# Performance work log

Hardware: AMD Instinct MI355X
Metric: run time of the kernel (lower is better)

Reference implementation:

```python
import jax, jax.numpy as jnp
import numpy as np

N_NODES = 100000


def gcn_conv(x, src, dst, dinv, W, b):
    # PyG GCNConv: h = D^-1/2 (A+I) D^-1/2 (x W) + b
    h = x @ W                                   # [N, out]
    norm = dinv[src] * dinv[dst]                # [E'] edge weights
    msg = norm[:, None] * h[src]                # gather + scale
    agg = jax.ops.segment_sum(msg, dst, num_segments=x.shape[0])
    return agg + b


def setup_inputs() -> dict:
    key = jax.random.key(0)
    ks = jax.random.split(key, 8)
    x = jax.random.normal(ks[0], (N_NODES, 64), dtype=jnp.float32)
    edge_index = jax.random.randint(ks[1], (2, 1600000), 0, N_NODES, dtype=jnp.int32)
    s = 0.1
    return {
        "x": x,
        "edge_index": edge_index,
        "W1": jax.random.normal(ks[2], (64, 64), dtype=jnp.float32) * s,
        "b1": jnp.zeros((64,), dtype=jnp.float32),
        "W2": jax.random.normal(ks[3], (64, 32), dtype=jnp.float32) * s,
        "b2": jnp.zeros((32,), dtype=jnp.float32),
        "W3": jax.random.normal(ks[4], (32, 2), dtype=jnp.float32) * s,
        "b3": jnp.zeros((2,), dtype=jnp.float32),
    }


def reference(x, edge_index, W1, b1, W2, b2, W3, b3):
    n = x.shape[0]
    loop = jnp.arange(n, dtype=edge_index.dtype)
    src = jnp.concatenate([edge_index[0], loop])  # add self-loops
    dst = jnp.concatenate([edge_index[1], loop])
    deg = jax.ops.segment_sum(jnp.ones_like(dst, dtype=x.dtype), dst, num_segments=n)
    dinv = jnp.where(deg > 0, jax.lax.rsqrt(jnp.maximum(deg, 1.0)), 0.0)
    h = jax.nn.relu(gcn_conv(x, src, dst, dinv, W1, b1))
    h = jax.nn.relu(gcn_conv(h, src, dst, dinv, W2, b2))
    return gcn_conv(h, src, dst, dinv, W3, b3)
```

## Files before the change

kernel.cpp:

```cpp
#include <hip/hip_runtime.h>
#include <hip/hip_fp16.h>

#define N_NODES 100000
#define N_EDGES 1600000
#define BSHIFT 9
#define NBUCK ((N_NODES + 511) / 512)
#define BCAP 12288

__global__ void bucket1_kernel(const int* __restrict__ src, const int* __restrict__ dst,
                               int* __restrict__ gbcount, int* __restrict__ bbuf, int E) {
    __shared__ int hcnt[NBUCK];
    __shared__ int hbase[NBUCK];
    int t = threadIdx.x;
    for (int i = t; i < NBUCK; i += 256) hcnt[i] = 0;
    __syncthreads();
    int e0 = blockIdx.x * 2048 + t;
    int ss[8], dd[8];
#pragma unroll
    for (int u = 0; u < 8; u++) {
        int e = e0 + u * 256;
        if (e < E) {
            ss[u] = src[e];
            dd[u] = dst[e];
            atomicAdd(&hcnt[dd[u] >> BSHIFT], 1);
        } else {
            dd[u] = -1;
        }
    }
    __syncthreads();
    for (int i = t; i < NBUCK; i += 256) {
        int c = hcnt[i];
        hbase[i] = c ? atomicAdd(&gbcount[i], c) : 0;
        hcnt[i] = 0;
    }
    __syncthreads();
#pragma unroll
    for (int u = 0; u < 8; u++) {
        if (dd[u] >= 0) {
            int bk = dd[u] >> BSHIFT;
            int r = atomicAdd(&hcnt[bk], 1);
            bbuf[(size_t)bk * BCAP + hbase[bk] + r] = ss[u] | ((dd[u] & 511) << 17);
        }
    }
}

__global__ void scan196_kernel(const int* __restrict__ gbcount, int* __restrict__ gbase,
                               int* __restrict__ rowptrN, int E) {
    __shared__ int s[256];
    int t = threadIdx.x;
    int v = (t < NBUCK) ? gbcount[t] : 0;
    s[t] = v;
    __syncthreads();
    for (int off = 1; off < 256; off <<= 1) {
        int u = (t >= off) ? s[t - off] : 0;
        __syncthreads();
        s[t] += u;
        __syncthreads();
    }
    if (t < NBUCK) gbase[t] = s[t] - v;
    if (t == 0) *rowptrN = E;
}

__global__ __launch_bounds__(512)
void bucket2_kernel(const int* __restrict__ bbuf, const int* __restrict__ gbcount,
                    const int* __restrict__ gbase, int* __restrict__ rowptr,
                    float* __restrict__ dinv, int* __restrict__ eidx, int N) {
    int b = blockIdx.x;
    int base_node = b << BSHIFT;
    int nn = min(512, N - base_node);
    int t = threadIdx.x;
    __shared__ int s[512];
    __shared__ int cur[512];
    s[t] = 0;
    __syncthreads();
    int sz = gbcount[b];
    const int* eb = bbuf + (size_t)b * BCAP;
    for (int j = t; j < sz; j += 512) atomicAdd(&s[((unsigned)eb[j]) >> 17], 1);
    __syncthreads();
    int myc = s[t];
    if (t < nn) dinv[base_node + t] = rsqrtf((float)myc + 1.0f);
    __syncthreads();
    for (int off = 1; off < 512; off <<= 1) {
        int u = (t >= off) ? s[t - off] : 0;
        __syncthreads();
        s[t] += u;
        __syncthreads();
    }
    int rp = gbase[b] + s[t] - myc;
    if (t < nn) rowptr[base_node + t] = rp;
    cur[t] = rp;
    __syncthreads();
    for (int j = t; j < sz; j += 512) {
        int e = eb[j];
        int pos = atomicAdd(&cur[((unsigned)e) >> 17], 1);
        eidx[pos] = e & 0x1FFFF;
    }
}

__global__ void sortrow_wave(const int* __restrict__ rowptr, int* __restrict__ eidx, int n) {
    int g = (blockIdx.x * blockDim.x + threadIdx.x) >> 6;
    int lane = threadIdx.x & 63;
    if (g >= n) return;
    int start = rowptr[g];
    int end = rowptr[g + 1];
    int len = end - start;
    if (len <= 1) return;

    if (len <= 64) {
        int v = (lane < len) ? eidx[start + lane] : 0x7fffffff;
#pragma unroll
        for (int k = 2; k <= 64; k <<= 1) {
#pragma unroll
            for (int j = k >> 1; j > 0; j >>= 1) {
                int partner = __shfl_xor(v, j, 64);
                bool up = ((lane & k) == 0);
                bool keepMin = (((lane & j) == 0) == up);
                int mn = min(v, partner), mx = max(v, partner);
                v = keepMin ? mn : mx;
            }
        }
        if (lane < len) eidx[start + lane] = v;
    } else if (lane == 0) {
        for (int i = start + 1; i < end; i++) {
            int key = eidx[i];
            int j = i - 1;
            while (j >= start && eidx[j] > key) { eidx[j + 1] = eidx[j]; j--; }
            eidx[j + 1] = key;
        }
    }
}

template <int FIN, int FOUT>
__global__ __launch_bounds__(256, 2)
void gemm_tiled(const float* __restrict__ in, const float* __restrict__ W,
                const float* __restrict__ dinv, __half* __restrict__ out, int n) {
    constexpr int CG = FOUT / 4;
    constexpr int RG = 256 / CG;
    constexpr int TR = RG * 4;
    constexpr int LDA = FIN + 4;
    __shared__ float sIn[TR * LDA];
    __shared__ float sW[FIN * FOUT];

    for (int i = threadIdx.x; i < FIN * FOUT / 4; i += 256)
        ((float4*)sW)[i] = ((const float4*)W)[i];

    int r0 = blockIdx.x * TR;
    for (int i = threadIdx.x; i < TR * FIN / 4; i += 256) {
        int rr = i / (FIN / 4);
        int cc = i % (FIN / 4);
        int gr = r0 + rr;
        float4 v = (gr < n) ? ((const float4*)in)[(size_t)gr * (FIN / 4) + cc]
                            : make_float4(0.f, 0.f, 0.f, 0.f);
        *(float4*)&sIn[rr * LDA + cc * 4] = v;
    }
    __syncthreads();

    int tc = threadIdx.x % CG;
    int tr = threadIdx.x / CG;
    int rbase = tr * 4, cbase = tc * 4;
    float acc[4][4] = {};

#pragma unroll 2
    for (int k = 0; k < FIN; k += 4) {
        float4 a[4], b[4];
#pragma unroll
        for (int i = 0; i < 4; i++) a[i] = *(float4*)&sIn[(rbase + i) * LDA + k];
#pragma unroll
        for (int kk = 0; kk < 4; kk++) b[kk] = *(float4*)&sW[(k + kk) * FOUT + cbase];
#pragma unroll
        for (int i = 0; i < 4; i++) {
            acc[i][0] += a[i].x * b[0].x + a[i].y * b[1].x + a[i].z * b[2].x + a[i].w * b[3].x;
            acc[i][1] += a[i].x * b[0].y + a[i].y * b[1].y + a[i].z * b[2].y + a[i].w * b[3].y;
            acc[i][2] += a[i].x * b[0].z + a[i].y * b[1].z + a[i].z * b[2].z + a[i].w * b[3].z;
            acc[i][3] += a[i].x * b[0].w + a[i].y * b[1].w + a[i].z * b[2].w + a[i].w * b[3].w;
        }
    }

#pragma unroll
    for (int i = 0; i < 4; i++) {
        int gr = r0 + rbase + i;
        if (gr < n) {
            float dv = dinv[gr];
            union { __half h[4]; uint2 u; } pk;
            pk.h[0] = __float2half_rn(dv * acc[i][0]);
            pk.h[1] = __float2half_rn(dv * acc[i][1]);
            pk.h[2] = __float2half_rn(dv * acc[i][2]);
            pk.h[3] = __float2half_rn(dv * acc[i][3]);
            *(uint2*)&out[(size_t)gr * FOUT + cbase] = pk.u;
        }
    }
}

template <int FIN, int FOUT, bool OUT_HALF>
__global__ __launch_bounds__(256, 4)
void agg_gemm_kernel(const int* __restrict__ eidx, const int* __restrict__ rowptr,
                     const float* __restrict__ dinv, const __half* __restrict__ h,
                     const float* __restrict__ bias, const float* __restrict__ W,
                     void* __restrict__ outv, int n) {
    constexpr int L = 8;
    constexpr int PH = FIN / L;
    constexpr int NODES = 256 / L;
    constexpr int SVS = FIN + 1;
    using vh = _Float16 __attribute__((ext_vector_type(PH)));
    __shared__ float sW[FIN * FOUT];
    __shared__ float sv[NODES * SVS];

    for (int i = threadIdx.x; i < FIN * FOUT / 4; i += 256)
        ((float4*)sW)[i] = ((const float4*)W)[i];

    int g = (blockIdx.x * blockDim.x + threadIdx.x) / L;
    int lane = threadIdx.x % L;
    int slot = threadIdx.x / L;
    float di = 0.f;

    if (g < n) {
        int j = rowptr[g];
        int end = rowptr[g + 1];
        di = dinv[g];
        const __half* hb = h + lane * PH;

        float acc0[PH], acc1[PH];
#pragma unroll
        for (int q = 0; q < PH; q++) { acc0[q] = 0.f; acc1[q] = 0.f; }

        for (; j + 8 <= end; j += 8) {
            int s0 = eidx[j];
            int s1 = eidx[j + 1];
            int s2 = eidx[j + 2];
            int s3 = eidx[j + 3];
            int s4 = eidx[j + 4];
            int s5 = eidx[j + 5];
            int s6 = eidx[j + 6];
            int s7 = eidx[j + 7];
            vh v0 = *(const vh*)(hb + (size_t)s0 * FIN);
            vh v1 = *(const vh*)(hb + (size_t)s1 * FIN);
            vh v2 = *(const vh*)(hb + (size_t)s2 * FIN);
            vh v3 = *(const vh*)(hb + (size_t)s3 * FIN);
            vh v4 = *(const vh*)(hb + (size_t)s4 * FIN);
            vh v5 = *(const vh*)(hb + (size_t)s5 * FIN);
            vh v6 = *(const vh*)(hb + (size_t)s6 * FIN);
            vh v7 = *(const vh*)(hb + (size_t)s7 * FIN);
#pragma unroll
            for (int q = 0; q < PH; q++) {
                acc0[q] += (float)v0[q] + (float)v2[q];
                acc1[q] += (float)v1[q] + (float)v3[q];
                acc0[q] += (float)v4[q] + (float)v6[q];
                acc1[q] += (float)v5[q] + (float)v7[q];
            }
        }
        for (; j + 2 <= end; j += 2) {
            int s0 = eidx[j];
            int s1 = eidx[j + 1];
            vh v0 = *(const vh*)(hb + (size_t)s0 * FIN);
            vh v1 = *(const vh*)(hb + (size_t)s1 * FIN);
#pragma unroll
            for (int q = 0; q < PH; q++) { acc0[q] += (float)v0[q]; acc1[q] += (float)v1[q]; }
        }
        if (j < end) {
            vh v = *(const vh*)(hb + (size_t)eidx[j] * FIN);
#pragma unroll
            for (int q = 0; q < PH; q++) acc0[q] += (float)v[q];
        }

        vh sf = *(const vh*)(hb + (size_t)g * FIN);
        float* svn = &sv[slot * SVS + lane * PH];
#pragma unroll
        for (int q = 0; q < PH; q++) {
            float v = di * ((acc0[q] + acc1[q]) + (float)sf[q]) + bias[lane * PH + q];
            svn[q] = fmaxf(v, 0.f);
        }
    }
    __syncthreads();

    if (g < n) {
        const float* vn = &sv[slot * SVS];
        if constexpr (OUT_HALF) {
            constexpr int PC = FOUT / L;
            float o[PC] = {};
            for (int k = 0; k < FIN; k++) {
                float vk = vn[k];
                float4 w = *(const float4*)&sW[k * FOUT + lane * PC];
                o[0] += vk * w.x; o[1] += vk * w.y; o[2] += vk * w.z; o[3] += vk * w.w;
            }
            union { __half h[4]; uint2 u; } pk;
#pragma unroll
            for (int q = 0; q < PC; q++) pk.h[q] = __float2half_rn(di * o[q]);
            *(uint2*)((__half*)outv + (size_t)g * FOUT + lane * PC) = pk.u;
        } else {
            if (lane < FOUT) {
                float o = 0.f;
                for (int k = 0; k < FIN; k++) o += vn[k] * sW[k * FOUT + lane];
                ((float*)outv)[(size_t)g * FOUT + lane] = di * o;
            }
        }
    }
}

template <int F>
__global__ void agg_kernel(const int* __restrict__ eidx, const int* __restrict__ rowptr,
                           const float* __restrict__ dinv, const float* __restrict__ h,
                           const float* __restrict__ b, float* __restrict__ out, int n) {
    int g = (blockIdx.x * blockDim.x + threadIdx.x) / F;
    int lane = threadIdx.x % F;
    if (g >= n) return;
    int j = rowptr[g];
    int end = rowptr[g + 1];
    float di = dinv[g];
    float hs = h[(size_t)g * F + lane];

    float acc0 = 0.f, acc1 = 0.f, acc2 = 0.f, acc3 = 0.f;
    float acc4 = 0.f, acc5 = 0.f, acc6 = 0.f, acc7 = 0.f;
    for (; j + 8 <= end; j += 8) {
        int s0 = eidx[j];
        int s1 = eidx[j + 1];
        int s2 = eidx[j + 2];
        int s3 = eidx[j + 3];
        int s4 = eidx[j + 4];
        int s5 = eidx[j + 5];
        int s6 = eidx[j + 6];
        int s7 = eidx[j + 7];
        acc0 += h[(size_t)s0 * F + lane];
        acc1 += h[(size_t)s1 * F + lane];
        acc2 += h[(size_t)s2 * F + lane];
        acc3 += h[(size_t)s3 * F + lane];
        acc4 += h[(size_t)s4 * F + lane];
        acc5 += h[(size_t)s5 * F + lane];
        acc6 += h[(size_t)s6 * F + lane];
        acc7 += h[(size_t)s7 * F + lane];
    }
    for (; j + 2 <= end; j += 2) {
        int s0 = eidx[j];
        int s1 = eidx[j + 1];
        acc0 += h[(size_t)s0 * F + lane];
        acc1 += h[(size_t)s1 * F + lane];
    }
    if (j < end) {
        acc2 += h[(size_t)eidx[j] * F + lane];
    }
    float acc = ((acc0 + acc1) + (acc2 + acc3)) + ((acc4 + acc5) + (acc6 + acc7));
    out[(size_t)g * F + lane] = di * (acc + hs) + b[lane];
}

extern "C" void kernel_launch(void* const* d_in, const int* in_sizes, int n_in,
                              void* d_out, int out_size, void* d_ws, size_t ws_size,
                              hipStream_t stream) {
    const float* x  = (const float*)d_in[0];
    const int* ei   = (const int*)d_in[1];
    const float* W1 = (const float*)d_in[2];
    const float* b1 = (const float*)d_in[3];
    const float* W2 = (const float*)d_in[4];
    const float* b2 = (const float*)d_in[5];
    const float* W3 = (const float*)d_in[6];
    const float* b3 = (const float*)d_in[7];
    float* out = (float*)d_out;

    const int N = N_NODES;
    const int E = N_EDGES;
    const int* src = ei;
    const int* dst = ei + E;

    char* p = (char*)d_ws;
    int*    rowptr  = (int*)p;            p += ((size_t)(N + 1) * 4 + 15) / 16 * 16;
    float*  dinv    = (float*)p;          p += ((size_t)N * 4 + 15) / 16 * 16;
    int*    gbcount = (int*)p;            p += ((size_t)NBUCK * 4 + 15) / 16 * 16;
    int*    gbase   = (int*)p;            p += ((size_t)NBUCK * 4 + 15) / 16 * 16;
    int*    eidx    = (int*)p;            p += (size_t)E * 4;
    __half* A1      = (__half*)p;         p += (size_t)N * 64 * 2;
    __half* A2      = (__half*)p;         p += (size_t)N * 32 * 2;
    float*  A3      = (float*)p;          p += (size_t)N * 2 * 4;
    int*    bbuf    = (int*)p;

    const int T = 256;

    hipMemsetAsync(gbcount, 0, NBUCK * sizeof(int), stream);
    bucket1_kernel<<<(E + 2047) / 2048, T, 0, stream>>>(src, dst, gbcount, bbuf, E);
    scan196_kernel<<<1, 256, 0, stream>>>(gbcount, gbase, rowptr + N, E);
    bucket2_kernel<<<NBUCK, 512, 0, stream>>>(bbuf, gbcount, gbase, rowptr, dinv, eidx, N);
    sortrow_wave<<<(N * 64 + T - 1) / T, T, 0, stream>>>(rowptr, eidx, N);

    gemm_tiled<64, 64><<<(N + 63) / 64, T, 0, stream>>>(x, W1, dinv, A1, N);

    agg_gemm_kernel<64, 32, true><<<(N + 31) / 32, T, 0, stream>>>(
        eidx, rowptr, dinv, A1, b1, W2, A2, N);

    agg_gemm_kernel<32, 2, false><<<(N + 31) / 32, T, 0, stream>>>(
        eidx, rowptr, dinv, A2, b2, W3, A3, N);

    agg_kernel<2><<<(N * 2 + T - 1) / T, T, 0, stream>>>(eidx, rowptr, dinv, A3, b3, out, N);
}
```

Before: 266.8 us.

## Aggregate before first GEMM and fuse both layer GEMMs into one kernel

Uses associativity: layer 1 now aggregates dinv-scaled fp16 input features and applies W1 afterwards, instead of running a separate GEMM first. The x-to-fp16 conversion with dinv scaling is folded into bucket2, and a new kernel does aggregation, the W1 GEMM, bias plus ReLU, and the W2 GEMM in one pass. This drops the standalone gemm_tiled launch and one intermediate round trip. In exchange, x is rounded to fp16 before the matmul, and the new kernel holds more shared memory (W1+W2), which may lower occupancy.

```diff
diff --git a/kernel.cpp b/kernel.cpp
--- a/kernel.cpp
+++ b/kernel.cpp
@@ -64,13 +64,15 @@
 __global__ __launch_bounds__(512)
 void bucket2_kernel(const int* __restrict__ bbuf, const int* __restrict__ gbcount,
                     const int* __restrict__ gbase, int* __restrict__ rowptr,
-                    float* __restrict__ dinv, int* __restrict__ eidx, int N) {
+                    float* __restrict__ dinv, int* __restrict__ eidx,
+                    const float* __restrict__ x, __half* __restrict__ x16, int N) {
     int b = blockIdx.x;
     int base_node = b << BSHIFT;
     int nn = min(512, N - base_node);
     int t = threadIdx.x;
     __shared__ int s[512];
     __shared__ int cur[512];
+    __shared__ float sdinv[512];
     s[t] = 0;
     __syncthreads();
     int sz = gbcount[b];
@@ -78,7 +80,9 @@
     for (int j = t; j < sz; j += 512) atomicAdd(&s[((unsigned)eb[j]) >> 17], 1);
     __syncthreads();
     int myc = s[t];
-    if (t < nn) dinv[base_node + t] = rsqrtf((float)myc + 1.0f);
+    float dv = rsqrtf((float)myc + 1.0f);
+    sdinv[t] = dv;
+    if (t < nn) dinv[base_node + t] = dv;
     __syncthreads();
     for (int off = 1; off < 512; off <<= 1) {
         int u = (t >= off) ? s[t - off] : 0;
@@ -94,6 +98,17 @@
         int e = eb[j];
         int pos = atomicAdd(&cur[((unsigned)e) >> 17], 1);
         eidx[pos] = e & 0x1FFFF;
+    }
+    for (int i = t; i < nn * 16; i += 512) {
+        int r = i >> 4, c = i & 15;
+        float4 v = ((const float4*)x)[((size_t)(base_node + r)) * 16 + c];
+        float d = sdinv[r];
+        union { __half h[4]; uint2 u; } pk;
+        pk.h[0] = __float2half_rn(d * v.x);
+        pk.h[1] = __float2half_rn(d * v.y);
+        pk.h[2] = __float2half_rn(d * v.z);
+        pk.h[3] = __float2half_rn(d * v.w);
+        *(uint2*)&x16[((size_t)(base_node + r)) * 64 + c * 4] = pk.u;
     }
 }
 
@@ -130,64 +145,120 @@
     }
 }
 
-template <int FIN, int FOUT>
-__global__ __launch_bounds__(256, 2)
-void gemm_tiled(const float* __restrict__ in, const float* __restrict__ W,
-                const float* __restrict__ dinv, __half* __restrict__ out, int n) {
-    constexpr int CG = FOUT / 4;
-    constexpr int RG = 256 / CG;
-    constexpr int TR = RG * 4;
-    constexpr int LDA = FIN + 4;
-    __shared__ float sIn[TR * LDA];
-    __shared__ float sW[FIN * FOUT];
-
-    for (int i = threadIdx.x; i < FIN * FOUT / 4; i += 256)
-        ((float4*)sW)[i] = ((const float4*)W)[i];
-
-    int r0 = blockIdx.x * TR;
-    for (int i = threadIdx.x; i < TR * FIN / 4; i += 256) {
-        int rr = i / (FIN / 4);
-        int cc = i % (FIN / 4);
-        int gr = r0 + rr;
-        float4 v = (gr < n) ? ((const float4*)in)[(size_t)gr * (FIN / 4) + cc]
-                            : make_float4(0.f, 0.f, 0.f, 0.f);
-        *(float4*)&sIn[rr * LDA + cc * 4] = v;
-    }
-    __syncthreads();
-
-    int tc = threadIdx.x % CG;
-    int tr = threadIdx.x / CG;
-    int rbase = tr * 4, cbase = tc * 4;
-    float acc[4][4] = {};
-
-#pragma unroll 2
-    for (int k = 0; k < FIN; k += 4) {
-        float4 a[4], b[4];
-#pragma unroll
-        for (int i = 0; i < 4; i++) a[i] = *(float4*)&sIn[(rbase + i) * LDA + k];
-#pragma unroll
-        for (int kk = 0; kk < 4; kk++) b[kk] = *(float4*)&sW[(k + kk) * FOUT + cbase];
-#pragma unroll
-        for (int i = 0; i < 4; i++) {
-            acc[i][0] += a[i].x * b[0].x + a[i].y * b[1].x + a[i].z * b[2].x + a[i].w * b[3].x;
-            acc[i][1] += a[i].x * b[0].y + a[i].y * b[1].y + a[i].z * b[2].y + a[i].w * b[3].y;
-            acc[i][2] += a[i].x * b[0].z + a[i].y * b[1].z + a[i].z * b[2].z + a[i].w * b[3].z;
-            acc[i][3] += a[i].x * b[0].w + a[i].y * b[1].w + a[i].z * b[2].w + a[i].w * b[3].w;
-        }
-    }
-
-#pragma unroll
-    for (int i = 0; i < 4; i++) {
-        int gr = r0 + rbase + i;
-        if (gr < n) {
-            float dv = dinv[gr];
-            union { __half h[4]; uint2 u; } pk;
-            pk.h[0] = __float2half_rn(dv * acc[i][0]);
-            pk.h[1] = __float2half_rn(dv * acc[i][1]);
-            pk.h[2] = __float2half_rn(dv * acc[i][2]);
-            pk.h[3] = __float2half_rn(dv * acc[i][3]);
-            *(uint2*)&out[(size_t)gr * FOUT + cbase] = pk.u;
-        }
+__global__ __launch_bounds__(256, 4)
+void agg_gemm2x_kernel(const int* __restrict__ eidx, const int* __restrict__ rowptr,
+                       const float* __restrict__ dinv, const __half* __restrict__ h,
+                       const float* __restrict__ b1, const float* __restrict__ W1,
+                       const float* __restrict__ W2, __half* __restrict__ outA2, int n) {
+    constexpr int L = 8;
+    constexpr int PH = 8;
+    constexpr int NODES = 32;
+    constexpr int SVS = 65;
+    using vh = _Float16 __attribute__((ext_vector_type(8)));
+    __shared__ float sW1[64 * 64];
+    __shared__ float sW2[64 * 32];
+    __shared__ float su[NODES * SVS];
+
+    for (int i = threadIdx.x; i < 64 * 64 / 4; i += 256)
+        ((float4*)sW1)[i] = ((const float4*)W1)[i];
+    for (int i = threadIdx.x; i < 64 * 32 / 4; i += 256)
+        ((float4*)sW2)[i] = ((const float4*)W2)[i];
+
+    int g = (blockIdx.x * blockDim.x + threadIdx.x) / L;
+    int lane = threadIdx.x % L;
+    int slot = threadIdx.x / L;
+    float di = 0.f;
+
+    if (g < n) {
+        int j = rowptr[g];
+        int end = rowptr[g + 1];
+        di = dinv[g];
+        const __half* hb = h + lane * PH;
+
+        float acc0[PH], acc1[PH];
+#pragma unroll
+        for (int q = 0; q < PH; q++) { acc0[q] = 0.f; acc1[q] = 0.f; }
+
+        for (; j + 8 <= end; j += 8) {
+            int s0 = eidx[j];
+            int s1 = eidx[j + 1];
+            int s2 = eidx[j + 2];
+            int s3 = eidx[j + 3];
+            int s4 = eidx[j + 4];
+            int s5 = eidx[j + 5];
+            int s6 = eidx[j + 6];
+            int s7 = eidx[j + 7];
+            vh v0 = *(const vh*)(hb + (size_t)s0 * 64);
+            vh v1 = *(const vh*)(hb + (size_t)s1 * 64);
+            vh v2 = *(const vh*)(hb + (size_t)s2 * 64);
+            vh v3 = *(const vh*)(hb + (size_t)s3 * 64);
+            vh v4 = *(const vh*)(hb + (size_t)s4 * 64);
+            vh v5 = *(const vh*)(hb + (size_t)s5 * 64);
+            vh v6 = *(const vh*)(hb + (size_t)s6 * 64);
+            vh v7 = *(const vh*)(hb + (size_t)s7 * 64);
+#pragma unroll
+            for (int q = 0; q < PH; q++) {
+                acc0[q] += (float)v0[q] + (float)v2[q];
+                acc1[q] += (float)v1[q] + (float)v3[q];
+                acc0[q] += (float)v4[q] + (float)v6[q];
+                acc1[q] += (float)v5[q] + (float)v7[q];
+            }
+        }
+        for (; j + 2 <= end; j += 2) {
+            int s0 = eidx[j];
+            int s1 = eidx[j + 1];
+            vh v0 = *(const vh*)(hb + (size_t)s0 * 64);
+            vh v1 = *(const vh*)(hb + (size_t)s1 * 64);
+#pragma unroll
+            for (int q = 0; q < PH; q++) { acc0[q] += (float)v0[q]; acc1[q] += (float)v1[q]; }
+        }
+        if (j < end) {
+            vh v = *(const vh*)(hb + (size_t)eidx[j] * 64);
+#pragma unroll
+            for (int q = 0; q < PH; q++) acc0[q] += (float)v[q];
+        }
+
+        vh sf = *(const vh*)(hb + (size_t)g * 64);
+        float* sun = &su[slot * SVS + lane * PH];
+#pragma unroll
+        for (int q = 0; q < PH; q++)
+            sun[q] = (acc0[q] + acc1[q]) + (float)sf[q];
+    }
+    __syncthreads();
+
+    float v8[8] = {};
+    if (g < n) {
+        const float* un = &su[slot * SVS];
+        for (int k = 0; k < 64; k++) {
+            float uk = un[k];
+            float4 wa = *(const float4*)&sW1[k * 64 + lane * 8];
+            float4 wb = *(const float4*)&sW1[k * 64 + lane * 8 + 4];
+            v8[0] += uk * wa.x; v8[1] += uk * wa.y; v8[2] += uk * wa.z; v8[3] += uk * wa.w;
+            v8[4] += uk * wb.x; v8[5] += uk * wb.y; v8[6] += uk * wb.z; v8[7] += uk * wb.w;
+        }
+#pragma unroll
+        for (int q = 0; q < 8; q++) v8[q] = fmaxf(di * v8[q] + b1[lane * 8 + q], 0.f);
+    }
+    __syncthreads();
+    if (g < n) {
+        float* sun = &su[slot * SVS + lane * 8];
+#pragma unroll
+        for (int q = 0; q < 8; q++) sun[q] = v8[q];
+    }
+    __syncthreads();
+
+    if (g < n) {
+        const float* vn = &su[slot * SVS];
+        float o[4] = {};
+        for (int k = 0; k < 64; k++) {
+            float vk = vn[k];
+            float4 w = *(const float4*)&sW2[k * 32 + lane * 4];
+            o[0] += vk * w.x; o[1] += vk * w.y; o[2] += vk * w.z; o[3] += vk * w.w;
+        }
+        union { __half h[4]; uint2 u; } pk;
+#pragma unroll
+        for (int q = 0; q < 4; q++) pk.h[q] = __float2half_rn(di * o[q]);
+        *(uint2*)&outA2[(size_t)g * 32 + lane * 4] = pk.u;
     }
 }
 
@@ -365,7 +436,7 @@
     int*    gbcount = (int*)p;            p += ((size_t)NBUCK * 4 + 15) / 16 * 16;
     int*    gbase   = (int*)p;            p += ((size_t)NBUCK * 4 + 15) / 16 * 16;
     int*    eidx    = (int*)p;            p += (size_t)E * 4;
-    __half* A1      = (__half*)p;         p += (size_t)N * 64 * 2;
+    __half* x16     = (__half*)p;         p += (size_t)N * 64 * 2;
     __half* A2      = (__half*)p;         p += (size_t)N * 32 * 2;
     float*  A3      = (float*)p;          p += (size_t)N * 2 * 4;
     int*    bbuf    = (int*)p;
@@ -375,13 +446,12 @@
     hipMemsetAsync(gbcount, 0, NBUCK * sizeof(int), stream);
     bucket1_kernel<<<(E + 2047) / 2048, T, 0, stream>>>(src, dst, gbcount, bbuf, E);
     scan196_kernel<<<1, 256, 0, stream>>>(gbcount, gbase, rowptr + N, E);
-    bucket2_kernel<<<NBUCK, 512, 0, stream>>>(bbuf, gbcount, gbase, rowptr, dinv, eidx, N);
+    bucket2_kernel<<<NBUCK, 512, 0, stream>>>(bbuf, gbcount, gbase, rowptr, dinv, eidx,
+                                              x, x16, N);
     sortrow_wave<<<(N * 64 + T - 1) / T, T, 0, stream>>>(rowptr, eidx, N);
 
-    gemm_tiled<64, 64><<<(N + 63) / 64, T, 0, stream>>>(x, W1, dinv, A1, N);
-
-    agg_gemm_kernel<64, 32, true><<<(N + 31) / 32, T, 0, stream>>>(
-        eidx, rowptr, dinv, A1, b1, W2, A2, N);
+    agg_gemm2x_kernel<<<(N + 31) / 32, T, 0, stream>>>(
+        eidx, rowptr, dinv, x16, b1, W1, W2, A2, N);
 
     agg_gemm_kernel<32, 2, false><<<(N + 31) / 32, T, 0, stream>>>(
         eidx, rowptr, dinv, A2, b2, W3, A3, N);
```

New measurement: 266.9 us. About the same (+0.0%).
